# Performance work log

Hardware: AMD Instinct MI355X
Metric: run time of the kernel (lower is better)

Reference implementation:

```python
import jax, jax.numpy as jnp
import numpy as np

B, S, H, NH = 1, 2048, 4096, 32
HD = H // NH
INV_NORM = 1.0 / np.sqrt(HD)


def _alibi_slopes(n_heads):
    # standard Bloom ALiBi slopes
    closest_pow2 = 2 ** int(np.floor(np.log2(n_heads)))
    base = 2.0 ** (-(2.0 ** -(np.log2(closest_pow2) - 3)))
    slopes = base ** np.arange(1, closest_pow2 + 1)
    if closest_pow2 != n_heads:
        extra_base = 2.0 ** (-(2.0 ** -(np.log2(2 * closest_pow2) - 3)))
        extra = extra_base ** np.arange(1, 2 * (n_heads - closest_pow2) + 1, 2)
        slopes = np.concatenate([slopes, extra])
    return slopes.astype(np.float32)


def setup_inputs() -> dict:
    key = jax.random.key(0)
    ks = jax.random.split(key, 6)
    hidden_states = jax.random.normal(ks[0], (B, S, H), dtype=jnp.float32)
    residual = jax.random.normal(ks[1], (B, S, H), dtype=jnp.float32)
    # ALiBi bias: slopes[h] * position, shape [B*NH, 1, S]
    slopes = jnp.asarray(_alibi_slopes(NH))  # [NH]
    pos = jnp.arange(S, dtype=jnp.float32)  # [S]
    alibi = (slopes[:, None] * pos[None, :])[:, None, :]  # [NH,1,S]
    alibi = jnp.tile(alibi, (B, 1, 1))  # [B*NH,1,S]
    # causal mask: True = masked out
    attention_mask = ~jnp.tril(jnp.ones((S, S), dtype=bool))[None, None]  # [1,1,S,S]
    qkv_w = jax.random.normal(ks[2], (3 * H, H), dtype=jnp.float32) * 0.02
    qkv_b = jax.random.normal(ks[3], (3 * H,), dtype=jnp.float32) * 0.02
    dense_w = jax.random.normal(ks[4], (H, H), dtype=jnp.float32) * 0.02
    dense_b = jax.random.normal(ks[5], (H,), dtype=jnp.float32) * 0.02
    return {
        "hidden_states": hidden_states,
        "residual": residual,
        "alibi": alibi,
        "attention_mask": attention_mask,
        "qkv_w": qkv_w,
        "qkv_b": qkv_b,
        "dense_w": dense_w,
        "dense_b": dense_b,
    }


def reference(hidden_states, residual, alibi, attention_mask, qkv_w, qkv_b, dense_w, dense_b):
    b, s, h = hidden_states.shape
    fused = hidden_states @ qkv_w.T + qkv_b  # [B,S,3H]
    fused = fused.reshape(b, s, NH, 3, HD)  # per-head interleaved q,k,v
    q, k, v = fused[..., 0, :], fused[..., 1, :], fused[..., 2, :]  # [B,S,NH,HD]
    # scores = beta*alibi + inv_norm * q @ k^T
    scores = jnp.einsum("bqnd,bknd->bnqk", q, k) * INV_NORM
    scores = scores + alibi.reshape(b, NH, 1, s)  # broadcast over q
    scores = jnp.where(attention_mask, jnp.finfo(scores.dtype).min, scores)
    probs = jax.nn.softmax(scores.astype(jnp.float32), axis=-1)  # [B,NH,S,S]
    ctx = jnp.einsum("bnqk,bknd->bqnd", probs, v).reshape(b, s, h)
    out = ctx @ dense_w.T + dense_b
    return residual + out  # dropout_add with p=0 / eval mode
```

## Files before the change

### kernel.cpp

```cpp
#include <hip/hip_runtime.h>
#include <cstdint>
#include <cstddef>

typedef unsigned short u16;
typedef __attribute__((ext_vector_type(8))) __bf16 bf16x8;
typedef __attribute__((ext_vector_type(4))) float f32x4;

#define S_LEN   2048
#define H_DIM   4096
#define NH_N    32
#define HD_N    128
#define QK_LD   8192

__device__ __forceinline__ u16 f2b(float f) {
  union { float f; unsigned u; } v; v.f = f;
  unsigned r = v.u + 0x7fffu + ((v.u >> 16) & 1u);
  return (u16)(r >> 16);
}

__device__ __forceinline__ void gl2lds16(const void* g, void* l) {
  __builtin_amdgcn_global_load_lds((__attribute__((address_space(1))) void*)g,
                                   (__attribute__((address_space(3))) void*)l,
                                   16, 0, 0);
}

__global__ __launch_bounds__(256)
void cvt3_kernel(const float* __restrict__ s0, u16* __restrict__ d0, int n0,
                 const float* __restrict__ s1, u16* __restrict__ d1, int n1,
                 const float* __restrict__ s2, u16* __restrict__ d2, int n2,
                 int b0, int b1) {
  int blk = blockIdx.x;
  const float* src; u16* dst; int n; int base;
  if (blk < b0)      { src = s0; dst = d0; n = n0; base = blk; }
  else if (blk < b1) { src = s1; dst = d1; n = n1; base = blk - b0; }
  else               { src = s2; dst = d2; n = n2; base = blk - b1; }
  int i = base * 256 + threadIdx.x;
  if (i >= n) return;
  float4 a = ((const float4*)src)[i];
  union { u16 o[4]; ushort4 v; } u;
  u.o[0] = f2b(a.x); u.o[1] = f2b(a.y); u.o[2] = f2b(a.z); u.o[3] = f2b(a.w);
  ((ushort4*)dst)[i] = u.v;
}

template <int OUTF32>
__global__ __launch_bounds__(256, 2)
void gemm_kernel(const u16* __restrict__ A, const u16* __restrict__ B,
                 const float* __restrict__ bias, const float* __restrict__ resid,
                 u16* __restrict__ outQK, u16* __restrict__ outVT,
                 float* __restrict__ outF,
                 int M, int N, int K) {
  __shared__ __align__(16) u16 As[128 * 64];
  __shared__ __align__(16) u16 Bs[128 * 64];
  const int tid  = threadIdx.x;
  const int lane = tid & 63;
  const int wave = tid >> 6;
  const int l15  = lane & 15;
  const int quad = lane >> 4;
  const int m0 = blockIdx.y * 128;
  const int n0 = blockIdx.x * 128;
  const int wm = (wave & 1) * 64;
  const int wn = (wave >> 1) * 64;

  f32x4 acc[4][4] = {};

  int sRow[4], sCol[4];
#pragma unroll
  for (int it = 0; it < 4; ++it) {
    int slot = wave * 256 + it * 64 + lane;
    int row  = slot >> 3;
    int kc   = (slot & 7) ^ (row & 7);
    sRow[it] = row;
    sCol[it] = kc * 8;
  }
  const u16* Ag = A + (size_t)m0 * K;
  const u16* Bg = B + (size_t)n0 * K;

  for (int kb = 0; kb < K; kb += 64) {
#pragma unroll
    for (int it = 0; it < 4; ++it) {
      int base = (wave * 256 + it * 64) * 8;
      gl2lds16(Ag + (size_t)sRow[it] * K + kb + sCol[it], &As[base]);
      gl2lds16(Bg + (size_t)sRow[it] * K + kb + sCol[it], &Bs[base]);
    }
    __syncthreads();
#pragma unroll
    for (int s = 0; s < 2; ++s) {
      const int kc = s * 4 + quad;
      bf16x8 af[4], bfr[4];
#pragma unroll
      for (int i = 0; i < 4; ++i) {
        int ra = wm + i * 16 + l15;
        af[i]  = *(const bf16x8*)&As[(ra * 8 + (kc ^ (ra & 7))) * 8];
        int rb = wn + i * 16 + l15;
        bfr[i] = *(const bf16x8*)&Bs[(rb * 8 + (kc ^ (rb & 7))) * 8];
      }
#pragma unroll
      for (int i = 0; i < 4; ++i)
#pragma unroll
        for (int j = 0; j < 4; ++j)
          acc[i][j] = __builtin_amdgcn_mfma_f32_16x16x32_bf16(af[i], bfr[j], acc[i][j], 0, 0, 0);
    }
    __syncthreads();
  }

#pragma unroll
  for (int i = 0; i < 4; ++i) {
    int rowb = m0 + wm + i * 16 + quad * 4;
#pragma unroll
    for (int j = 0; j < 4; ++j) {
      int c0 = n0 + wn + j * 16;
      float bb = bias[c0 + l15];
      if (OUTF32) {
#pragma unroll
        for (int r = 0; r < 4; ++r) {
          size_t rowoff = (size_t)(rowb + r) * N;
          outF[rowoff + c0 + l15] = acc[i][j][r] + bb + resid[rowoff + c0 + l15];
        }
      } else {
        int head = c0 / 384;
        int rem  = c0 % 384;
        int part = rem >> 7;
        if (part == 2) {
          int d = (rem & 127) + l15;
          union { ushort4 v; u16 e[4]; } pk;
#pragma unroll
          for (int r = 0; r < 4; ++r) pk.e[r] = f2b(acc[i][j][r] + bb);
          *(ushort4*)&outVT[(size_t)head * (HD_N * S_LEN) + (size_t)d * S_LEN + rowb] = pk.v;
        } else {
          int colq = head * 256 + part * 128 + (rem & 127) + l15;
#pragma unroll
          for (int r = 0; r < 4; ++r)
            outQK[(size_t)(rowb + r) * QK_LD + colq] = f2b(acc[i][j][r] + bb);
        }
      }
    }
  }
}

__global__ __launch_bounds__(512, 4)
void attn_kernel(const u16* __restrict__ QK, const u16* __restrict__ VT,
                 const float* __restrict__ alibi, u16* __restrict__ CTX) {
  __shared__ __align__(16) u16 Ks[2][64 * 128];
  __shared__ __align__(16) u16 Vs[2][128 * 64];
  __shared__ __align__(16) u16 Ps[8 * 1024];
  const int tid  = threadIdx.x;
  const int lane = tid & 63;
  const int wave = tid >> 6;
  const int l15  = lane & 15;
  const int quad = lane >> 4;
  const int lin  = blockIdx.x;
  const int ub   = lin & 255;
  const int vb   = lin >> 8;
  const int head = ub & 31;
  const int idx  = ub >> 5;
  const int qt   = vb ? idx : (15 - idx);
  const int q0   = qt * 128;
  const float c1 = 0.08838834764831845f * 1.4426950408889634f;
  const float slope2 = alibi[head * S_LEN + 1] * 1.4426950408889634f;

  const u16* Kbase = QK + head * 256 + 128;
  const u16* Vbase = VT + (size_t)head * (HD_N * S_LEN);

  int kRow[2], kCol[2], vRow[2], vCol[2], sBase[2];
#pragma unroll
  for (int it = 0; it < 2; ++it) {
    int slot = it * 512 + tid;
    int kr = slot >> 4;
    kRow[it] = kr;
    kCol[it] = ((slot & 15) ^ (kr & 15)) * 8;
    int d = slot >> 3;
    vRow[it] = d;
    vCol[it] = ((slot & 7) ^ (d & 7)) * 8;
    sBase[it] = (it * 512 + wave * 64) * 8;
  }

  bf16x8 qf[4];
  {
    const u16* qp = QK + (size_t)(q0 + wave * 16 + l15) * QK_LD + head * 256;
#pragma unroll
    for (int s = 0; s < 4; ++s) qf[s] = *(const bf16x8*)(qp + s * 32 + quad * 8);
  }

  float m_i[4], l_i[4];
#pragma unroll
  for (int r = 0; r < 4; ++r) { m_i[r] = -3.0e38f; l_i[r] = 0.0f; }
  f32x4 acc[8] = {};

  const int nk = 2 * qt + 2;

#pragma unroll
  for (int it = 0; it < 2; ++it) {
    gl2lds16(Kbase + (size_t)kRow[it] * QK_LD + kCol[it], &Ks[0][sBase[it]]);
    gl2lds16(Vbase + (size_t)vRow[it] * S_LEN + vCol[it], &Vs[0][sBase[it]]);
  }
  __syncthreads();

  int cur = 0;
  for (int kt = 0; kt < nk; ++kt) {
    const int k0 = kt * 64;
    if (kt + 1 < nk) {
      const int kn = k0 + 64;
#pragma unroll
      for (int it = 0; it < 2; ++it) {
        gl2lds16(Kbase + (size_t)(kn + kRow[it]) * QK_LD + kCol[it], &Ks[cur ^ 1][sBase[it]]);
        gl2lds16(Vbase + (size_t)vRow[it] * S_LEN + kn + vCol[it], &Vs[cur ^ 1][sBase[it]]);
      }
    }

    f32x4 sc[4] = {};
    __builtin_amdgcn_s_setprio(1);
#pragma unroll
    for (int s = 0; s < 4; ++s) {
      const int kc = s * 4 + quad;
      bf16x8 kf[4];
#pragma unroll
      for (int j = 0; j < 4; ++j) {
        int row = j * 16 + l15;
        kf[j] = *(const bf16x8*)&Ks[cur][(row * 16 + (kc ^ (row & 15))) * 8];
      }
#pragma unroll
      for (int j = 0; j < 4; ++j)
        sc[j] = __builtin_amdgcn_mfma_f32_16x16x32_bf16(qf[s], kf[j], sc[j], 0, 0, 0);
    }
    __builtin_amdgcn_s_setprio(0);

    const bool maskT = (kt >= 2 * qt);
    float xv[4][4];
    float mt[4] = { -3.0e38f, -3.0e38f, -3.0e38f, -3.0e38f };
#pragma unroll
    for (int j = 0; j < 4; ++j) {
      int key  = k0 + j * 16 + l15;
      float al = slope2 * (float)key;
#pragma unroll
      for (int r = 0; r < 4; ++r) {
        float x = sc[j][r] * c1 + al;
        if (maskT) {
          int qrow = q0 + wave * 16 + quad * 4 + r;
          if (key > qrow) x = -3.0e38f;
        }
        xv[j][r] = x;
        mt[r] = fmaxf(mt[r], x);
      }
    }
#pragma unroll
    for (int r = 0; r < 4; ++r) {
      float v = mt[r];
      v = fmaxf(v, __shfl_xor(v, 1));
      v = fmaxf(v, __shfl_xor(v, 2));
      v = fmaxf(v, __shfl_xor(v, 4));
      v = fmaxf(v, __shfl_xor(v, 8));
      mt[r] = fmaxf(m_i[r], v);
    }
    float alpha[4], psum[4];
#pragma unroll
    for (int r = 0; r < 4; ++r) {
      alpha[r] = exp2f(m_i[r] - mt[r]);
      m_i[r] = mt[r];
      psum[r] = 0.0f;
    }
#pragma unroll
    for (int j = 0; j < 4; ++j) {
      int col = j * 16 + l15;
      int kc  = col >> 3;
#pragma unroll
      for (int r = 0; r < 4; ++r) {
        float p = exp2f(xv[j][r] - m_i[r]);
        psum[r] += p;
        int qrow = quad * 4 + r;
        Ps[wave * 1024 + (qrow * 8 + (kc ^ (qrow & 7))) * 8 + (col & 7)] = f2b(p);
      }
    }
#pragma unroll
    for (int r = 0; r < 4; ++r) {
      float v = psum[r];
      v += __shfl_xor(v, 1);
      v += __shfl_xor(v, 2);
      v += __shfl_xor(v, 4);
      v += __shfl_xor(v, 8);
      l_i[r] = l_i[r] * alpha[r] + v;
    }
#pragma unroll
    for (int t = 0; t < 8; ++t)
#pragma unroll
      for (int r = 0; r < 4; ++r) acc[t][r] *= alpha[r];

    __builtin_amdgcn_s_setprio(1);
#pragma unroll
    for (int s = 0; s < 2; ++s) {
      const int kc = s * 4 + quad;
      bf16x8 pf = *(const bf16x8*)&Ps[wave * 1024 + (l15 * 8 + (kc ^ (l15 & 7))) * 8];
#pragma unroll
      for (int t = 0; t < 8; ++t) {
        int row = t * 16 + l15;
        bf16x8 vf = *(const bf16x8*)&Vs[cur][(row * 8 + (kc ^ (row & 7))) * 8];
        acc[t] = __builtin_amdgcn_mfma_f32_16x16x32_bf16(pf, vf, acc[t], 0, 0, 0);
      }
    }
    __builtin_amdgcn_s_setprio(0);
    __syncthreads();
    cur ^= 1;
  }

#pragma unroll
  for (int r = 0; r < 4; ++r) {
    float inv = 1.0f / l_i[r];
    size_t rowoff = (size_t)(q0 + wave * 16 + quad * 4 + r) * H_DIM;
#pragma unroll
    for (int t = 0; t < 8; ++t)
      CTX[rowoff + head * HD_N + t * 16 + l15] = f2b(acc[t][r] * inv);
  }
}

extern "C" void kernel_launch(void* const* d_in, const int* in_sizes, int n_in,
                              void* d_out, int out_size, void* d_ws, size_t ws_size,
                              hipStream_t stream) {
  const float* hidden   = (const float*)d_in[0];
  const float* residual = (const float*)d_in[1];
  const float* alibi    = (const float*)d_in[2];
  const float* qkv_w    = (const float*)d_in[4];
  const float* qkv_b    = (const float*)d_in[5];
  const float* dense_w  = (const float*)d_in[6];
  const float* dense_b  = (const float*)d_in[7];
  float* out = (float*)d_out;

  u16* Xb  = (u16*)d_ws;
  u16* Wq  = Xb + (size_t)S_LEN * H_DIM;
  u16* Wd  = Wq + (size_t)3 * H_DIM * H_DIM;
  u16* QKb = Wd + (size_t)H_DIM * H_DIM;
  u16* VT  = QKb + (size_t)S_LEN * QK_LD;
  u16* CTX = VT + (size_t)NH_N * HD_N * S_LEN;

  {
    int n0 = S_LEN * H_DIM / 4;
    int n1 = 3 * H_DIM * H_DIM / 4;
    int n2 = H_DIM * H_DIM / 4;
    int nb0 = (n0 + 255) / 256, nb1 = (n1 + 255) / 256, nb2 = (n2 + 255) / 256;
    cvt3_kernel<<<dim3(nb0 + nb1 + nb2), 256, 0, stream>>>(
        hidden, Xb, n0, qkv_w, Wq, n1, dense_w, Wd, n2, nb0, nb0 + nb1);
  }

  gemm_kernel<0><<<dim3(3 * H_DIM / 128, S_LEN / 128), 256, 0, stream>>>(
      Xb, Wq, qkv_b, nullptr, QKb, VT, nullptr, S_LEN, 3 * H_DIM, H_DIM);

  attn_kernel<<<dim3(512), 512, 0, stream>>>(QKb, VT, alibi, CTX);

  gemm_kernel<1><<<dim3(H_DIM / 128, S_LEN / 128), 256, 0, stream>>>(
      CTX, Wd, dense_b, residual, nullptr, nullptr, out, S_LEN, H_DIM, H_DIM);
}
```

Baseline: 775.9 us.

## Rewrite GEMMs as 256x128 tile, 8-wave, triple-buffered LDS pipeline

Both projection GEMMs now use a 512-thread kernel with 256x128 output tiles and three LDS buffers filled by async global-to-LDS loads two k-steps ahead. Waits use explicit vmcnt instead of full syncthreads, and the MFMA blocks run at raised wave priority. A workgroup index swizzle groups neighbouring tiles to improve L2 reuse. The goal is to hide global load latency behind MFMA work and raise arithmetic intensity per tile. The cost is 144KB of LDS per block, which may limit occupancy below the requested two blocks, and the hand-written waitcnt logic is fragile.

```diff
diff --git a/kernel.cpp b/kernel.cpp
--- a/kernel.cpp
+++ b/kernel.cpp
@@ -11,6 +11,8 @@
 #define NH_N    32
 #define HD_N    128
 #define QK_LD   8192
+
+#define WAIT_VM(N) asm volatile("s_waitcnt vmcnt(" #N ")" ::: "memory")
 
 __device__ __forceinline__ u16 f2b(float f) {
   union { float f; unsigned u; } v; v.f = f;
@@ -43,72 +45,117 @@
 }
 
 template <int OUTF32>
-__global__ __launch_bounds__(256, 2)
-void gemm_kernel(const u16* __restrict__ A, const u16* __restrict__ B,
-                 const float* __restrict__ bias, const float* __restrict__ resid,
-                 u16* __restrict__ outQK, u16* __restrict__ outVT,
-                 float* __restrict__ outF,
-                 int M, int N, int K) {
-  __shared__ __align__(16) u16 As[128 * 64];
-  __shared__ __align__(16) u16 Bs[128 * 64];
+__global__ __launch_bounds__(512, 2)
+void gemm8_kernel(const u16* __restrict__ A, const u16* __restrict__ B,
+                  const float* __restrict__ bias, const float* __restrict__ resid,
+                  u16* __restrict__ outQK, u16* __restrict__ outVT,
+                  float* __restrict__ outF,
+                  int M, int N, int K) {
+  __shared__ __align__(16) u16 sm[3 * 24576];
   const int tid  = threadIdx.x;
   const int lane = tid & 63;
   const int wave = tid >> 6;
   const int l15  = lane & 15;
   const int quad = lane >> 4;
-  const int m0 = blockIdx.y * 128;
-  const int n0 = blockIdx.x * 128;
-  const int wm = (wave & 1) * 64;
-  const int wn = (wave >> 1) * 64;
+  const int wr   = wave >> 1;
+  const int wc   = wave & 1;
+
+  const int gx  = gridDim.x;
+  const int nwg = gx * gridDim.y;
+  const int lin = blockIdx.y * gx + blockIdx.x;
+  const int swz = (lin & 7) * (nwg >> 3) + (lin >> 3);
+  const int m0  = (swz / gx) * 256;
+  const int n0  = (swz % gx) * 128;
 
   f32x4 acc[4][4] = {};
 
-  int sRow[4], sCol[4];
-#pragma unroll
-  for (int it = 0; it < 4; ++it) {
-    int slot = wave * 256 + it * 64 + lane;
+  int aRow[2], aCol[2];
+#pragma unroll
+  for (int it = 0; it < 2; ++it) {
+    int slot = it * 512 + tid;
     int row  = slot >> 3;
-    int kc   = (slot & 7) ^ (row & 7);
-    sRow[it] = row;
-    sCol[it] = kc * 8;
-  }
+    aRow[it] = row;
+    aCol[it] = ((slot & 7) ^ (row & 7)) * 8;
+  }
+  int bRow, bCol;
+  { int row = tid >> 3; bRow = row; bCol = ((tid & 7) ^ (row & 7)) * 8; }
+  const int aBase = wave * 64 * 8;
+  const int bBase = wave * 64 * 8;
+
   const u16* Ag = A + (size_t)m0 * K;
   const u16* Bg = B + (size_t)n0 * K;
 
-  for (int kb = 0; kb < K; kb += 64) {
-#pragma unroll
-    for (int it = 0; it < 4; ++it) {
-      int base = (wave * 256 + it * 64) * 8;
-      gl2lds16(Ag + (size_t)sRow[it] * K + kb + sCol[it], &As[base]);
-      gl2lds16(Bg + (size_t)sRow[it] * K + kb + sCol[it], &Bs[base]);
-    }
-    __syncthreads();
-#pragma unroll
-    for (int s = 0; s < 2; ++s) {
-      const int kc = s * 4 + quad;
-      bf16x8 af[4], bfr[4];
+  const int NT = K >> 6;
+
+#define STAGE_TILE(BSEL, KB)                                                  \
+  {                                                                           \
+    u16* as_ = sm + (BSEL) * 24576;                                           \
+    u16* bs_ = as_ + 16384;                                                   \
+    _Pragma("unroll")                                                         \
+    for (int h = 0; h < 2; ++h) {                                             \
+      _Pragma("unroll")                                                       \
+      for (int it = 0; it < 2; ++it)                                          \
+        gl2lds16(Ag + (size_t)(h * 128 + aRow[it]) * K + (KB) + aCol[it],     \
+                 as_ + h * 8192 + it * 4096 + aBase);                         \
+      gl2lds16(Bg + (size_t)(h * 64 + bRow) * K + (KB) + bCol,                \
+               bs_ + h * 4096 + bBase);                                       \
+    }                                                                         \
+  }
+
+  STAGE_TILE(0, 0);
+  STAGE_TILE(1, 64);
+
+  for (int kt = 0; kt < NT; ++kt) {
+    const int cur = kt % 3;
+    const u16* as = sm + cur * 24576 + (wr >> 1) * 8192;
+    const u16* bs = sm + cur * 24576 + 16384 + wc * 4096;
+    if (kt < NT - 1) { WAIT_VM(6); } else { WAIT_VM(0); }
+    __builtin_amdgcn_sched_barrier(0);
+    __builtin_amdgcn_s_barrier();
+    __builtin_amdgcn_sched_barrier(0);
+    const int rbase = (wr & 1) * 64;
+#pragma unroll
+    for (int ks = 0; ks < 2; ++ks) {
+      if (kt + 2 < NT) {
+        const int kb = (kt + 2) << 6;
+        u16* asn = sm + ((kt + 2) % 3) * 24576;
+        u16* bsn = asn + 16384;
+#pragma unroll
+        for (int it = 0; it < 2; ++it)
+          gl2lds16(Ag + (size_t)(ks * 128 + aRow[it]) * K + kb + aCol[it],
+                   asn + ks * 8192 + it * 4096 + aBase);
+        gl2lds16(Bg + (size_t)(ks * 64 + bRow) * K + kb + bCol,
+                 bsn + ks * 4096 + bBase);
+      }
+      const int kcq = ks * 4 + quad;
+      bf16x8 af[4], bf[4];
 #pragma unroll
       for (int i = 0; i < 4; ++i) {
-        int ra = wm + i * 16 + l15;
-        af[i]  = *(const bf16x8*)&As[(ra * 8 + (kc ^ (ra & 7))) * 8];
-        int rb = wn + i * 16 + l15;
-        bfr[i] = *(const bf16x8*)&Bs[(rb * 8 + (kc ^ (rb & 7))) * 8];
-      }
+        int ra = rbase + i * 16 + l15;
+        af[i] = *(const bf16x8*)&as[(ra * 8 + (kcq ^ (ra & 7))) * 8];
+        int rb = i * 16 + l15;
+        bf[i] = *(const bf16x8*)&bs[(rb * 8 + (kcq ^ (rb & 7))) * 8];
+      }
+      __builtin_amdgcn_s_setprio(1);
 #pragma unroll
       for (int i = 0; i < 4; ++i)
 #pragma unroll
         for (int j = 0; j < 4; ++j)
-          acc[i][j] = __builtin_amdgcn_mfma_f32_16x16x32_bf16(af[i], bfr[j], acc[i][j], 0, 0, 0);
-    }
-    __syncthreads();
-  }
+          acc[i][j] = __builtin_amdgcn_mfma_f32_16x16x32_bf16(af[i], bf[j], acc[i][j], 0, 0, 0);
+      __builtin_amdgcn_s_setprio(0);
+    }
+    __builtin_amdgcn_sched_barrier(0);
+    __builtin_amdgcn_s_barrier();
+    __builtin_amdgcn_sched_barrier(0);
+  }
+#undef STAGE_TILE
 
 #pragma unroll
   for (int i = 0; i < 4; ++i) {
-    int rowb = m0 + wm + i * 16 + quad * 4;
+    int rowb = m0 + wr * 64 + i * 16 + quad * 4;
 #pragma unroll
     for (int j = 0; j < 4; ++j) {
-      int c0 = n0 + wn + j * 16;
+      int c0 = n0 + wc * 64 + j * 16;
       float bb = bias[c0 + l15];
       if (OUTF32) {
 #pragma unroll
@@ -339,11 +386,11 @@
         hidden, Xb, n0, qkv_w, Wq, n1, dense_w, Wd, n2, nb0, nb0 + nb1);
   }
 
-  gemm_kernel<0><<<dim3(3 * H_DIM / 128, S_LEN / 128), 256, 0, stream>>>(
+  gemm8_kernel<0><<<dim3(3 * H_DIM / 128, S_LEN / 256), 512, 0, stream>>>(
       Xb, Wq, qkv_b, nullptr, QKb, VT, nullptr, S_LEN, 3 * H_DIM, H_DIM);
 
   attn_kernel<<<dim3(512), 512, 0, stream>>>(QKb, VT, alibi, CTX);
 
-  gemm_kernel<1><<<dim3(H_DIM / 128, S_LEN / 128), 256, 0, stream>>>(
+  gemm8_kernel<1><<<dim3(H_DIM / 128, S_LEN / 256), 512, 0, stream>>>(
       CTX, Wd, dense_b, residual, nullptr, nullptr, out, S_LEN, H_DIM, H_DIM);
 }
```

New measurement: 737.2 us. 5.0% less time.
